# Performance work log

Measured on AMD Instinct MI355X. Metric: run time of the kernel, lower is better.

Reference implementation:

```python
import jax, jax.numpy as jnp
import numpy as np

B, H, W, C = 4, 64, 64, 512
D = C // 8  # 64


def setup_inputs() -> dict:
    key = jax.random.key(0)
    ks = jax.random.split(key, 5)
    s_in = 1.0 / np.sqrt(C)
    s_out = 1.0 / np.sqrt(D)
    return {
        "x": jax.random.normal(ks[0], (B, H, W, C), dtype=jnp.float32),
        "Wq": jax.random.normal(ks[1], (C, D), dtype=jnp.float32) * s_in,
        "bq": jnp.zeros((D,), dtype=jnp.float32),
        "Wk": jax.random.normal(ks[2], (C, D), dtype=jnp.float32) * s_in,
        "bk": jnp.zeros((D,), dtype=jnp.float32),
        "Wv": jax.random.normal(ks[3], (C, D), dtype=jnp.float32) * s_in,
        "bv": jnp.zeros((D,), dtype=jnp.float32),
        "Wo": jax.random.normal(ks[4], (D, C), dtype=jnp.float32) * s_out,
        "bo": jnp.zeros((C,), dtype=jnp.float32),
    }


def reference(x, Wq, bq, Wk, bk, Wv, bv, Wo, bo):
    b, h, w, c = x.shape
    d = c // 8
    n = h * w
    # 1x1 convs == per-pixel matmuls; relu applied as in the original
    q = jax.nn.relu(jnp.einsum('bhwc,cd->bhwd', x, Wq) + bq).reshape(b, n, d)
    k = jax.nn.relu(jnp.einsum('bhwc,cd->bhwd', x, Wk) + bk).reshape(b, n, d)
    v = jax.nn.relu(jnp.einsum('bhwc,cd->bhwd', x, Wv) + bv).reshape(b, n, d)
    # unscaled attention: softmax(Q K^T) over the key axis (last axis)
    scores = jnp.einsum('bnd,bmd->bnm', q, k)  # [B, N, N]
    attn = jax.nn.softmax(scores, axis=-1)
    out = jnp.einsum('bnm,bmd->bnd', attn, v)  # [B, N, D]
    out = out.reshape(b, h, w, d)
    # output 1x1 conv back to C channels, then relu
    out = jax.nn.relu(jnp.einsum('bhwd,dc->bhwc', out, Wo) + bo)
    return out
```

## Files before the change

kernel.cpp:

```cpp
#include <hip/hip_runtime.h>
#include <math.h>

typedef float    f32x4  __attribute__((ext_vector_type(4)));
typedef __bf16   bf16x8 __attribute__((ext_vector_type(8)));
typedef _Float16 half8  __attribute__((ext_vector_type(8)));
typedef unsigned short ushort_t;
typedef unsigned short ushort8 __attribute__((ext_vector_type(8)));

#define NTOK  4096
#define CD    512
#define DD    64
#define BQ    256
#define BK    64
#define KSTR  72
#define PSTR  68
#define NROWS 16384
#define LOG2E 1.4426950408889634f

#define MFMAH(a, b, c) __builtin_amdgcn_mfma_f32_16x16x32_f16((a), (b), (c), 0, 0, 0)
#define MFMAB(a, b, c) __builtin_amdgcn_mfma_f32_16x16x32_bf16((a), (b), (c), 0, 0, 0)
#define EXP2(x) __builtin_amdgcn_exp2f(x)

static __device__ __forceinline__ ushort_t f2h(float f) {
    union { _Float16 h; ushort_t u; } a; a.h = (_Float16)f; return a.u;
}
static __device__ __forceinline__ ushort_t f2bf(float f) {
    union { __bf16 h; ushort_t u; } a; a.h = (__bf16)f; return a.u;
}

__global__ __launch_bounds__(256) void wprep_kernel(
    const float* __restrict__ Wq, const float* __restrict__ Wk,
    const float* __restrict__ Wv, const float* __restrict__ Wo,
    ushort_t* __restrict__ wqk, ushort_t* __restrict__ wv_t,
    ushort_t* __restrict__ woT)
{
    const int idx = blockIdx.x * 256 + threadIdx.x;
    if (idx < 192*512) {
        const int col = idx >> 9;
        const int k   = idx & 511;
        const float* W = (col < 64) ? Wq : (col < 128 ? Wk : Wv);
        const int c = col & 63;
        float wv = W[(size_t)k*DD + c];
        if (col < 64) wv *= LOG2E;
        if (col < 128) wqk[(size_t)col*CD + k] = f2h(wv);
        else           wv_t[(size_t)(col - 128)*CD + k] = f2h(wv);
    } else {
        const int i = idx - 192*512;
        const int c = i >> 6, d = i & 63;
        woT[i] = f2h(Wo[(size_t)d*CD + c]);
    }
}

__global__ __launch_bounds__(256) void qkv_gemm(
    const float* __restrict__ x,
    const ushort_t* __restrict__ wqk, const ushort_t* __restrict__ wv_t,
    const float* __restrict__ bq, const float* __restrict__ bk,
    const float* __restrict__ bv,
    ushort_t* __restrict__ qf, ushort_t* __restrict__ kf,
    ushort_t* __restrict__ vT)
{
    __shared__ __align__(16) ushort_t xs_s [32*72];
    __shared__ __align__(16) ushort_t wqk_s[128*72];
    __shared__ __align__(16) ushort_t wv_s [64*72];
    __shared__ __align__(16) ushort_t vtile[64*40];

    const int tid  = threadIdx.x;
    const int w    = tid >> 6;
    const int lane = tid & 63;
    const int l15  = lane & 15;
    const int l4   = lane >> 4;
    const int r0   = blockIdx.x * 32;

    const int rf = w & 1;
    const int cg = w >> 1;

    f32x4 acc[6];
    #pragma unroll
    for (int j = 0; j < 6; ++j) acc[j] = (f32x4){0.f,0.f,0.f,0.f};

    const int xrow = tid >> 3, xk = (tid & 7) * 8;
    const int wcol = tid >> 1, wk = (tid & 1) * 32;
    const int vcol = tid >> 2, vk = (tid & 3) * 16;

    f32x4   px0, px1;
    ushort8 pw[4], pwv[2];

    {
        const float* xp = &x[(size_t)(r0 + xrow)*CD + xk];
        px0 = *(const f32x4*)xp;  px1 = *(const f32x4*)(xp + 4);
        const ushort_t* hp = &wqk[(size_t)wcol*CD + wk];
        #pragma unroll
        for (int i = 0; i < 4; ++i) pw[i] = *(const ushort8*)(hp + 8*i);
        const ushort_t* vp = &wv_t[(size_t)vcol*CD + vk];
        pwv[0] = *(const ushort8*)vp;  pwv[1] = *(const ushort8*)(vp + 8);
    }

    for (int kt = 0; kt < 8; ++kt) {
        __syncthreads();
        {
            ushort8 h8;
            #pragma unroll
            for (int i = 0; i < 8; ++i)
                h8[i] = f2h((i < 4) ? px0[i] : px1[i-4]);
            *(ushort8*)&xs_s[xrow*72 + xk] = h8;
        }
        #pragma unroll
        for (int i = 0; i < 4; ++i)
            *(ushort8*)&wqk_s[wcol*72 + wk + 8*i] = pw[i];
        *(ushort8*)&wv_s[vcol*72 + vk]     = pwv[0];
        *(ushort8*)&wv_s[vcol*72 + vk + 8] = pwv[1];

        if (kt + 1 < 8) {
            const int ko = (kt + 1) * 64;
            const float* xp = &x[(size_t)(r0 + xrow)*CD + ko + xk];
            px0 = *(const f32x4*)xp;  px1 = *(const f32x4*)(xp + 4);
            const ushort_t* hp = &wqk[(size_t)wcol*CD + ko + wk];
            #pragma unroll
            for (int i = 0; i < 4; ++i) pw[i] = *(const ushort8*)(hp + 8*i);
            const ushort_t* vp = &wv_t[(size_t)vcol*CD + ko + vk];
            pwv[0] = *(const ushort8*)vp;  pwv[1] = *(const ushort8*)(vp + 8);
        }
        __syncthreads();

        #pragma unroll
        for (int k32 = 0; k32 < 2; ++k32) {
            const int ao = (rf*16 + l15)*72 + 8*l4 + 32*k32;
            half8 ax = *(const half8*)&xs_s[ao];
            #pragma unroll
            for (int j = 0; j < 6; ++j) {
                const int cf = 6*cg + j;
                if (cf < 8) {
                    const int bo = (16*cf + l15)*72 + 8*l4 + 32*k32;
                    half8 bw = *(const half8*)&wqk_s[bo];
                    acc[j] = MFMAH(ax, bw, acc[j]);
                } else {
                    const int bo = ((cf-8)*16 + l15)*72 + 8*l4 + 32*k32;
                    half8 bw = *(const half8*)&wv_s[bo];
                    acc[j] = MFMAH(ax, bw, acc[j]);
                }
            }
        }
    }

    #pragma unroll
    for (int j = 0; j < 6; ++j) {
        const int cf = 6*cg + j;
        const int col16 = cf*16 + l15;
        if (cf < 4) {
            const float bias = bq[col16] * LOG2E;
            #pragma unroll
            for (int r = 0; r < 4; ++r) {
                const size_t row = (size_t)(r0 + rf*16 + 4*l4 + r);
                qf[row*DD + col16] = f2h(fmaxf(acc[j][r] + bias, 0.f));
            }
        } else if (cf < 8) {
            const int kc = col16 - 64;
            const float bias = bk[kc];
            #pragma unroll
            for (int r = 0; r < 4; ++r) {
                const size_t row = (size_t)(r0 + rf*16 + 4*l4 + r);
                kf[row*DD + kc] = f2h(fmaxf(acc[j][r] + bias, 0.f));
            }
        } else {
            const int d = col16 - 128;
            const float bias = bv[d];
            #pragma unroll
            for (int r = 0; r < 4; ++r)
                vtile[d*40 + rf*16 + 4*l4 + r] =
                    f2bf(fmaxf(acc[j][r] + bias, 0.f));
        }
    }
    __syncthreads();
    {
        const int d  = tid >> 2;
        const int j8 = (tid & 3) * 8;
        const int bb   = r0 / NTOK;
        const int tok0 = r0 % NTOK;
        ushort8 vv = *(const ushort8*)&vtile[d*40 + j8];
        *(ushort8*)&vT[((size_t)bb*DD + d)*NTOK + tok0 + j8] = vv;
    }
}

__global__ __launch_bounds__(256, 2) void attn_kernel(
    const ushort_t* __restrict__ qf, const ushort_t* __restrict__ kf,
    const ushort_t* __restrict__ vT,
    ushort_t* __restrict__ o_part, float* __restrict__ l_part, int nseg)
{
    __shared__ __align__(16) ushort_t kf_s[BK*KSTR];
    __shared__ __align__(16) ushort_t vt_s[DD*KSTR];
    __shared__ __align__(16) ushort_t p_s [BQ*PSTR];

    const int tid  = threadIdx.x;
    const int w    = tid >> 6;
    const int lane = tid & 63;
    const int l15  = lane & 15;
    const int l4   = lane >> 4;

    const int p    = blockIdx.x;
    const int seg  = p % nseg;
    const int rest = p / nseg;
    const int qb   = rest & (NTOK/BQ - 1);
    const int b    = rest / (NTOK/BQ);
    const int kv0  = seg * (NTOK / nseg);
    const int tiles = (NTOK / nseg) / BK;

    half8 qfr[4][2];
    #pragma unroll
    for (int u = 0; u < 4; ++u) {
        const size_t qrow = ((size_t)b*NTOK + (size_t)qb*BQ + 64*w + 16*u + l15)*DD;
        #pragma unroll
        for (int s = 0; s < 2; ++s)
            qfr[u][s] = *(const half8*)&qf[qrow + 8*l4 + 32*s];
    }

    f32x4 acc[4][4];
    float l_run[4][4];
    #pragma unroll
    for (int u = 0; u < 4; ++u)
        #pragma unroll
        for (int nt = 0; nt < 4; ++nt) {
            acc[u][nt] = (f32x4){0.f,0.f,0.f,0.f};
            l_run[u][nt] = 0.f;
        }

    const int skey = tid >> 2;
    const int sc   = (tid & 3) * 16;
    const size_t kst = (size_t)b*NTOK*DD + (size_t)skey*DD + sc;
    const size_t vst = (size_t)b*DD*NTOK + (size_t)skey*NTOK + sc;

    ushort8 rgk0, rgk1, rgv0, rgv1;
    rgk0 = *(const ushort8*)&kf[kst + (size_t)kv0*DD];
    rgk1 = *(const ushort8*)&kf[kst + (size_t)kv0*DD + 8];
    rgv0 = *(const ushort8*)&vT[vst + kv0];
    rgv1 = *(const ushort8*)&vT[vst + kv0 + 8];

    for (int t = 0; t < tiles; ++t) {
        __syncthreads();
        *(ushort8*)&kf_s[skey*KSTR + sc]     = rgk0;
        *(ushort8*)&kf_s[skey*KSTR + sc + 8] = rgk1;
        *(ushort8*)&vt_s[skey*KSTR + sc]     = rgv0;
        *(ushort8*)&vt_s[skey*KSTR + sc + 8] = rgv1;
        if (t + 1 < tiles) {
            const size_t ko = (size_t)(kv0 + (t+1)*BK);
            rgk0 = *(const ushort8*)&kf[kst + ko*DD];
            rgk1 = *(const ushort8*)&kf[kst + ko*DD + 8];
            rgv0 = *(const ushort8*)&vT[vst + ko];
            rgv1 = *(const ushort8*)&vT[vst + ko + 8];
        }
        __syncthreads();

        half8 kfr[2][4];
        #pragma unroll
        for (int s = 0; s < 2; ++s)
            #pragma unroll
            for (int nt = 0; nt < 4; ++nt)
                kfr[s][nt] = *(const half8*)&kf_s[(16*nt + l15)*KSTR + 8*l4 + 32*s];

        #pragma unroll
        for (int u = 0; u < 4; ++u) {
            f32x4 sv[4];
            #pragma unroll
            for (int nt = 0; nt < 4; ++nt) sv[nt] = (f32x4){0.f,0.f,0.f,0.f};
            #pragma unroll
            for (int s = 0; s < 2; ++s)
                #pragma unroll
                for (int nt = 0; nt < 4; ++nt)
                    sv[nt] = MFMAH(qfr[u][s], kfr[s][nt], sv[nt]);
            #pragma unroll
            for (int r = 0; r < 4; ++r) {
                float s0 = EXP2(sv[0][r]);
                float s1 = EXP2(sv[1][r]);
                float s2 = EXP2(sv[2][r]);
                float s3 = EXP2(sv[3][r]);
                sv[0][r] = s0; sv[1][r] = s1;
                sv[2][r] = s2; sv[3][r] = s3;
                l_run[u][r] += (s0 + s1) + (s2 + s3);
            }
            #pragma unroll
            for (int nt = 0; nt < 4; ++nt)
                #pragma unroll
                for (int r = 0; r < 4; ++r)
                    p_s[(64*w + 16*u + 4*l4 + r)*PSTR + 16*nt + l15] =
                        f2bf(sv[nt][r]);
        }

        bf16x8 vfr[2][4];
        #pragma unroll
        for (int s = 0; s < 2; ++s)
            #pragma unroll
            for (int nt = 0; nt < 4; ++nt)
                vfr[s][nt] = *(const bf16x8*)&vt_s[(16*nt + l15)*KSTR + 8*l4 + 32*s];
        #pragma unroll
        for (int u = 0; u < 4; ++u) {
            bf16x8 paf0 = *(const bf16x8*)&p_s[(64*w + 16*u + l15)*PSTR + 8*l4];
            bf16x8 paf1 = *(const bf16x8*)&p_s[(64*w + 16*u + l15)*PSTR + 8*l4 + 32];
            #pragma unroll
            for (int nt = 0; nt < 4; ++nt) {
                acc[u][nt] = MFMAB(paf0, vfr[0][nt], acc[u][nt]);
                acc[u][nt] = MFMAB(paf1, vfr[1][nt], acc[u][nt]);
            }
        }
    }

    const size_t prow0 = (size_t)(seg*4 + b)*NTOK + (size_t)qb*BQ + 64*w;
    #pragma unroll
    for (int u = 0; u < 4; ++u)
        #pragma unroll
        for (int r = 0; r < 4; ++r) {
            float ls = l_run[u][r];
            ls += __shfl_xor(ls, 1);
            ls += __shfl_xor(ls, 2);
            ls += __shfl_xor(ls, 4);
            ls += __shfl_xor(ls, 8);
            const size_t row = prow0 + 16*u + 4*l4 + r;
            #pragma unroll
            for (int nt = 0; nt < 4; ++nt)
                o_part[row*DD + 16*nt + l15] = f2bf(acc[u][nt][r]);
            if (l15 == 0) l_part[row] = ls;
        }
}

__global__ __launch_bounds__(256) void oproj_gemm(
    const ushort_t* __restrict__ o_part, const float* __restrict__ l_part,
    const ushort_t* __restrict__ woT, const float* __restrict__ bo,
    float* __restrict__ out, int nseg)
{
    const int tid  = threadIdx.x;
    const int w    = tid >> 6;
    const int lane = tid & 63;
    const int l15  = lane & 15;
    const int l4   = lane >> 4;
    const int r0   = blockIdx.x * 32;
    const int rf   = w & 1;
    const int cg   = w >> 1;

    const int row = r0 + rf*16 + l15;
    float lsum = 0.f;
    for (int s = 0; s < nseg; ++s)
        lsum += l_part[(size_t)s*NROWS + row];
    const float inv = 1.0f / lsum;

    f32x4 acc[16];
    #pragma unroll
    for (int j = 0; j < 16; ++j) acc[j] = (f32x4){0.f,0.f,0.f,0.f};

    #pragma unroll
    for (int ks = 0; ks < 2; ++ks) {
        const int k0 = 8*l4 + 32*ks;
        float ov[8] = {0.f,0.f,0.f,0.f,0.f,0.f,0.f,0.f};
        for (int s = 0; s < nseg; ++s) {
            const bf16x8 a = *(const bf16x8*)
                &o_part[((size_t)s*NROWS + row)*DD + k0];
            #pragma unroll
            for (int i = 0; i < 8; ++i) ov[i] += (float)a[i];
        }
        half8 ah;
        #pragma unroll
        for (int i = 0; i < 8; ++i)
            ah[i] = (_Float16)(ov[i] * inv);
        #pragma unroll
        for (int j = 0; j < 16; ++j) {
            const int cf = cg*16 + j;
            const half8 bfr = *(const half8*)&woT[(size_t)(16*cf + l15)*DD + k0];
            acc[j] = MFMAH(ah, bfr, acc[j]);
        }
    }

    #pragma unroll
    for (int j = 0; j < 16; ++j) {
        const int col  = (cg*16 + j)*16 + l15;
        const float bias = bo[col];
        #pragma unroll
        for (int r = 0; r < 4; ++r)
            out[(size_t)(r0 + rf*16 + 4*l4 + r)*CD + col] =
                fmaxf(acc[j][r] + bias, 0.f);
    }
}

extern "C" void kernel_launch(void* const* d_in, const int* in_sizes, int n_in,
                              void* d_out, int out_size, void* d_ws, size_t ws_size,
                              hipStream_t stream) {
    const float* x  = (const float*)d_in[0];
    const float* Wq = (const float*)d_in[1];
    const float* bq = (const float*)d_in[2];
    const float* Wk = (const float*)d_in[3];
    const float* bk = (const float*)d_in[4];
    const float* Wv = (const float*)d_in[5];
    const float* bv = (const float*)d_in[6];
    const float* Wo = (const float*)d_in[7];
    const float* bo = (const float*)d_in[8];
    float* out = (float*)d_out;

    ushort_t* u = (ushort_t*)d_ws;
    const size_t SEG = (size_t)NROWS * DD;
    ushort_t* qf  = u;
    ushort_t* kf  = u + SEG;
    ushort_t* vT  = u + 2*SEG;

    ushort_t* wqk  = u + 3*SEG;
    ushort_t* wv_t = wqk + 128*512;
    ushort_t* woT  = wv_t + 64*512;
    ushort_t* o_part = woT + 512*64;

    const size_t base_b  = (3*SEG + 192*512 + 512*64) * sizeof(ushort_t);
    const size_t per_seg = (size_t)NROWS*DD*2 + (size_t)NROWS*4;
    int nseg = 1;
    if      (ws_size >= base_b + 8*per_seg) nseg = 8;
    else if (ws_size >= base_b + 4*per_seg) nseg = 4;
    else if (ws_size >= base_b + 2*per_seg) nseg = 2;
    float* l_part = (float*)(o_part + (size_t)nseg*NROWS*DD);

    wprep_kernel<<<512, 256, 0, stream>>>(Wq, Wk, Wv, Wo, wqk, wv_t, woT);
    qkv_gemm<<<NROWS/32, 256, 0, stream>>>(x, wqk, wv_t,
                                           bq, bk, bv, qf, kf, vT);
    attn_kernel<<<(NTOK/BQ) * 4 * nseg, 256, 0, stream>>>(
        qf, kf, vT, o_part, l_part, nseg);
    oproj_gemm<<<NROWS/32, 256, 0, stream>>>(o_part, l_part, woT,
                                             bo, out, nseg);
}
```

Measured before the change: 71.88 us.

## Drop LDS staging in QKV GEMM, load MFMA fragments directly from global

Rewrites the QKV projection kernel so each wave loads its x and weight fragments straight from global memory into registers instead of staging tiles through shared memory with double buffering and two barriers per k-step. Each wave now covers both 16-row fragments for three 16-column output groups, reusing one weight fragment for two MFMAs. This removes the LDS writes, LDS reads and block-wide syncs. In exchange, x rows are re-read by all four waves and the loads are less coalesced and no longer prefetched, so the kernel relies on cache hits to hide global latency.

```diff
diff --git a/kernel.cpp b/kernel.cpp
--- a/kernel.cpp
+++ b/kernel.cpp
@@ -59,9 +59,6 @@
     ushort_t* __restrict__ qf, ushort_t* __restrict__ kf,
     ushort_t* __restrict__ vT)
 {
-    __shared__ __align__(16) ushort_t xs_s [32*72];
-    __shared__ __align__(16) ushort_t wqk_s[128*72];
-    __shared__ __align__(16) ushort_t wv_s [64*72];
     __shared__ __align__(16) ushort_t vtile[64*40];
 
     const int tid  = threadIdx.x;
@@ -71,103 +68,70 @@
     const int l4   = lane >> 4;
     const int r0   = blockIdx.x * 32;
 
-    const int rf = w & 1;
-    const int cg = w >> 1;
-
-    f32x4 acc[6];
-    #pragma unroll
-    for (int j = 0; j < 6; ++j) acc[j] = (f32x4){0.f,0.f,0.f,0.f};
-
-    const int xrow = tid >> 3, xk = (tid & 7) * 8;
-    const int wcol = tid >> 1, wk = (tid & 1) * 32;
-    const int vcol = tid >> 2, vk = (tid & 3) * 16;
-
-    f32x4   px0, px1;
-    ushort8 pw[4], pwv[2];
-
-    {
-        const float* xp = &x[(size_t)(r0 + xrow)*CD + xk];
-        px0 = *(const f32x4*)xp;  px1 = *(const f32x4*)(xp + 4);
-        const ushort_t* hp = &wqk[(size_t)wcol*CD + wk];
-        #pragma unroll
-        for (int i = 0; i < 4; ++i) pw[i] = *(const ushort8*)(hp + 8*i);
-        const ushort_t* vp = &wv_t[(size_t)vcol*CD + vk];
-        pwv[0] = *(const ushort8*)vp;  pwv[1] = *(const ushort8*)(vp + 8);
-    }
-
-    for (int kt = 0; kt < 8; ++kt) {
-        __syncthreads();
-        {
-            ushort8 h8;
-            #pragma unroll
-            for (int i = 0; i < 8; ++i)
-                h8[i] = f2h((i < 4) ? px0[i] : px1[i-4]);
-            *(ushort8*)&xs_s[xrow*72 + xk] = h8;
-        }
-        #pragma unroll
-        for (int i = 0; i < 4; ++i)
-            *(ushort8*)&wqk_s[wcol*72 + wk + 8*i] = pw[i];
-        *(ushort8*)&wv_s[vcol*72 + vk]     = pwv[0];
-        *(ushort8*)&wv_s[vcol*72 + vk + 8] = pwv[1];
-
-        if (kt + 1 < 8) {
-            const int ko = (kt + 1) * 64;
-            const float* xp = &x[(size_t)(r0 + xrow)*CD + ko + xk];
-            px0 = *(const f32x4*)xp;  px1 = *(const f32x4*)(xp + 4);
-            const ushort_t* hp = &wqk[(size_t)wcol*CD + ko + wk];
-            #pragma unroll
-            for (int i = 0; i < 4; ++i) pw[i] = *(const ushort8*)(hp + 8*i);
-            const ushort_t* vp = &wv_t[(size_t)vcol*CD + ko + vk];
-            pwv[0] = *(const ushort8*)vp;  pwv[1] = *(const ushort8*)(vp + 8);
-        }
-        __syncthreads();
-
-        #pragma unroll
-        for (int k32 = 0; k32 < 2; ++k32) {
-            const int ao = (rf*16 + l15)*72 + 8*l4 + 32*k32;
-            half8 ax = *(const half8*)&xs_s[ao];
-            #pragma unroll
-            for (int j = 0; j < 6; ++j) {
-                const int cf = 6*cg + j;
-                if (cf < 8) {
-                    const int bo = (16*cf + l15)*72 + 8*l4 + 32*k32;
-                    half8 bw = *(const half8*)&wqk_s[bo];
-                    acc[j] = MFMAH(ax, bw, acc[j]);
-                } else {
-                    const int bo = ((cf-8)*16 + l15)*72 + 8*l4 + 32*k32;
-                    half8 bw = *(const half8*)&wv_s[bo];
-                    acc[j] = MFMAH(ax, bw, acc[j]);
-                }
+    f32x4 acc[2][3];
+    #pragma unroll
+    for (int rf = 0; rf < 2; ++rf)
+        #pragma unroll
+        for (int j = 0; j < 3; ++j) acc[rf][j] = (f32x4){0.f,0.f,0.f,0.f};
+
+    for (int ks = 0; ks < 16; ++ks) {
+        const int k0 = 32*ks + 8*l4;
+        half8 af[2];
+        #pragma unroll
+        for (int rf = 0; rf < 2; ++rf) {
+            const float* xp = &x[(size_t)(r0 + rf*16 + l15)*CD + k0];
+            const f32x4 a0 = *(const f32x4*)xp;
+            const f32x4 a1 = *(const f32x4*)(xp + 4);
+            #pragma unroll
+            for (int i = 0; i < 4; ++i) {
+                af[rf][i]     = (_Float16)a0[i];
+                af[rf][i + 4] = (_Float16)a1[i];
             }
         }
-    }
-
-    #pragma unroll
-    for (int j = 0; j < 6; ++j) {
-        const int cf = 6*cg + j;
+        #pragma unroll
+        for (int j = 0; j < 3; ++j) {
+            const int cf = 3*w + j;
+            const ushort_t* wp = (cf < 8)
+                ? &wqk [(size_t)(16*cf + l15)*CD + k0]
+                : &wv_t[(size_t)(16*(cf-8) + l15)*CD + k0];
+            const half8 bw = *(const half8*)wp;
+            acc[0][j] = MFMAH(af[0], bw, acc[0][j]);
+            acc[1][j] = MFMAH(af[1], bw, acc[1][j]);
+        }
+    }
+
+    #pragma unroll
+    for (int j = 0; j < 3; ++j) {
+        const int cf = 3*w + j;
         const int col16 = cf*16 + l15;
         if (cf < 4) {
             const float bias = bq[col16] * LOG2E;
             #pragma unroll
-            for (int r = 0; r < 4; ++r) {
-                const size_t row = (size_t)(r0 + rf*16 + 4*l4 + r);
-                qf[row*DD + col16] = f2h(fmaxf(acc[j][r] + bias, 0.f));
-            }
+            for (int rf = 0; rf < 2; ++rf)
+                #pragma unroll
+                for (int r = 0; r < 4; ++r) {
+                    const size_t row = (size_t)(r0 + rf*16 + 4*l4 + r);
+                    qf[row*DD + col16] = f2h(fmaxf(acc[rf][j][r] + bias, 0.f));
+                }
         } else if (cf < 8) {
             const int kc = col16 - 64;
             const float bias = bk[kc];
             #pragma unroll
-            for (int r = 0; r < 4; ++r) {
-                const size_t row = (size_t)(r0 + rf*16 + 4*l4 + r);
-                kf[row*DD + kc] = f2h(fmaxf(acc[j][r] + bias, 0.f));
-            }
+            for (int rf = 0; rf < 2; ++rf)
+                #pragma unroll
+                for (int r = 0; r < 4; ++r) {
+                    const size_t row = (size_t)(r0 + rf*16 + 4*l4 + r);
+                    kf[row*DD + kc] = f2h(fmaxf(acc[rf][j][r] + bias, 0.f));
+                }
         } else {
             const int d = col16 - 128;
             const float bias = bv[d];
             #pragma unroll
-            for (int r = 0; r < 4; ++r)
-                vtile[d*40 + rf*16 + 4*l4 + r] =
-                    f2bf(fmaxf(acc[j][r] + bias, 0.f));
+            for (int rf = 0; rf < 2; ++rf)
+                #pragma unroll
+                for (int r = 0; r < 4; ++r)
+                    vtile[d*40 + rf*16 + 4*l4 + r] =
+                        f2bf(fmaxf(acc[rf][j][r] + bias, 0.f));
         }
     }
     __syncthreads();
```

New measurement: 86.31 us. 20.1% more time.
